# Performance work log

Measured on AMD Instinct MI355X. Metric: run time of the kernel, lower is better.

## Reference

```python
import jax, jax.numpy as jnp
import numpy as np

D_MODEL = 1024
D_STATE = 16
D_CONV = 4
EXPAND = 2
D_INNER = EXPAND * D_MODEL          # 2048
DT_RANK = (D_MODEL + 15) // 16      # 64 (mamba 'auto')
B, L = 2, 1024


def _mamba_params(key, scale=0.02):
    ks = jax.random.split(key, 6)
    return dict(
        inW=jax.random.normal(ks[0], (2 * D_INNER, D_MODEL), jnp.float32) * scale,
        convW=jax.random.normal(ks[1], (D_INNER, 1, D_CONV), jnp.float32) * scale,
        convb=jnp.zeros((D_INNER,), jnp.float32),
        xprojW=jax.random.normal(ks[2], (DT_RANK + 2 * D_STATE, D_INNER), jnp.float32) * scale,
        dtW=jax.random.normal(ks[3], (D_INNER, DT_RANK), jnp.float32) * scale,
        dtb=jax.random.normal(ks[4], (D_INNER,), jnp.float32) * scale,
        A_log=jnp.log(jnp.tile(jnp.arange(1, D_STATE + 1, dtype=jnp.float32), (D_INNER, 1))),
        Dskip=jnp.ones((D_INNER,), jnp.float32),
        outW=jax.random.normal(ks[5], (D_MODEL, D_INNER), jnp.float32) * scale,
    )


def setup_inputs() -> dict:
    key = jax.random.key(0)
    kx, kf, kb, kp = jax.random.split(key, 4)
    inp = {"x": jax.random.normal(kx, (B, L, D_MODEL), jnp.float32)}
    inp["ln_w"] = jnp.ones((D_MODEL,), jnp.float32)
    inp["ln_b"] = jnp.zeros((D_MODEL,), jnp.float32)
    for pref, k in (("f_", kf), ("b_", kb)):
        for name, v in _mamba_params(k).items():
            inp[pref + name] = v
    inp["proj_W"] = jax.random.normal(kp, (D_MODEL, 2 * D_MODEL), jnp.float32) * 0.02
    inp["proj_b"] = jnp.zeros((D_MODEL,), jnp.float32)
    return inp


def _layernorm(x, w, b, eps=1e-5):
    mu = jnp.mean(x, axis=-1, keepdims=True)
    var = jnp.var(x, axis=-1, keepdims=True)
    return (x - mu) * jax.lax.rsqrt(var + eps) * w + b


def _mamba(x, inW, convW, convb, xprojW, dtW, dtb, A_log, Dskip, outW):
    # x: [B, L, d_model]
    xz = jnp.einsum('bld,ed->ble', x, inW)           # [B,L,2*d_inner]
    xs, z = jnp.split(xz, 2, axis=-1)                # each [B,L,d_inner]
    # depthwise causal conv over L
    xc = jnp.transpose(xs, (0, 2, 1))                # [B,d_inner,L]
    xc = jax.lax.conv_general_dilated(
        xc, convW, window_strides=(1,), padding=[(D_CONV - 1, 0)],
        feature_group_count=D_INNER)
    xs = jax.nn.silu(jnp.transpose(xc + convb[None, :, None], (0, 2, 1)))
    # input-dependent dt, B, C
    xdb = jnp.einsum('bld,ed->ble', xs, xprojW)      # [B,L,dt_rank+2*d_state]
    dt, Bm, Cm = jnp.split(xdb, [DT_RANK, DT_RANK + D_STATE], axis=-1)
    dt = jax.nn.softplus(jnp.einsum('blr,dr->bld', dt, dtW) + dtb)  # [B,L,d_inner]
    A = -jnp.exp(A_log)                              # [d_inner,d_state], negative
    dA = jnp.exp(dt[..., None] * A)                  # [B,L,d_inner,d_state]
    dBx = dt[..., None] * Bm[:, :, None, :] * xs[..., None]

    def step(h, inputs):
        dA_t, dBx_t, C_t = inputs                    # [B,d,s],[B,d,s],[B,s]
        h = h * dA_t + dBx_t
        y = jnp.einsum('bds,bs->bd', h, C_t)
        return h, y

    h0 = jnp.zeros((x.shape[0], D_INNER, D_STATE), x.dtype)
    _, ys = jax.lax.scan(step, h0, (jnp.moveaxis(dA, 1, 0),
                                    jnp.moveaxis(dBx, 1, 0),
                                    jnp.moveaxis(Cm, 1, 0)))
    y = jnp.moveaxis(ys, 0, 1)                       # [B,L,d_inner]
    y = (y + xs * Dskip) * jax.nn.silu(z)
    return jnp.einsum('bld,ed->ble', y, outW)        # [B,L,d_model]


def reference(x, ln_w, ln_b,
              f_inW, f_convW, f_convb, f_xprojW, f_dtW, f_dtb, f_A_log, f_Dskip, f_outW,
              b_inW, b_convW, b_convb, b_xprojW, b_dtW, b_dtb, b_A_log, b_Dskip, b_outW,
              proj_W, proj_b):
    normed = _layernorm(x, ln_w, ln_b)
    fwd_out = _mamba(normed, f_inW, f_convW, f_convb, f_xprojW, f_dtW, f_dtb,
                     f_A_log, f_Dskip, f_outW)
    bwd_out = _mamba(normed[:, ::-1, :], b_inW, b_convW, b_convb, b_xprojW, b_dtW,
                     b_dtb, b_A_log, b_Dskip, b_outW)[:, ::-1, :]
    combined = jnp.concatenate([fwd_out, bwd_out], axis=-1)
    return x + jnp.einsum('blc,ec->ble', combined, proj_W) + proj_b
```

## Files before the change

kernel.cpp:

```cpp
#include <hip/hip_runtime.h>
#include <hip/hip_bf16.h>
#include <math.h>

#define DM   1024
#define DI   2048
#define DTR  64
#define DST  16
#define NB   2
#define LL   1024
#define MR   (NB*LL)
#define XLD  128
#define KS   8

typedef __bf16 bf16x8 __attribute__((ext_vector_type(8)));
typedef float  f32x4  __attribute__((ext_vector_type(4)));
typedef unsigned short u16x8 __attribute__((ext_vector_type(8)));

__device__ __forceinline__ float siluf(float x) { return x / (1.f + __expf(-x)); }
__device__ __forceinline__ float softplusf(float x) {
    return fmaxf(x, 0.f) + log1pf(__expf(-fabsf(x)));
}
__device__ __forceinline__ unsigned short f2bf(float f) {
    __hip_bfloat16 h = __float2bfloat16(f);
    return *reinterpret_cast<unsigned short*>(&h);
}
__device__ __forceinline__ float bf2f(__hip_bfloat16 h) { return __bfloat162float(h); }
__device__ __forceinline__ float bfu2f(unsigned short u) {
    __hip_bfloat16 h = *reinterpret_cast<__hip_bfloat16*>(&u);
    return __bfloat162float(h);
}

__device__ __forceinline__ void gl2lds16(const __hip_bfloat16* g, __hip_bfloat16* l)
{
    __builtin_amdgcn_global_load_lds(
        (const __attribute__((address_space(1))) unsigned int*)g,
        (__attribute__((address_space(3))) unsigned int*)l, 16, 0, 0);
}

__global__ __launch_bounds__(256) void prep_k(
    const float* __restrict__ s0, const float* __restrict__ s1,
    const float* __restrict__ s2, const float* __restrict__ s3,
    const float* __restrict__ s4, __hip_bfloat16* __restrict__ warena,
    const float* __restrict__ fx, const float* __restrict__ bx,
    __hip_bfloat16* __restrict__ wpb2,
    const float* __restrict__ fo, const float* __restrict__ bo,
    __hip_bfloat16* __restrict__ wot,
    const float* __restrict__ x, const float* __restrict__ lnw,
    const float* __restrict__ lnb, __hip_bfloat16* __restrict__ nb)
{
    __shared__ float pshm[64 * 65];
    const int b = blockIdx.x;
    const int tid = threadIdx.x;

    if (b < 2624) {
        long base = (long)b * 4096;
        const float* src; long off;
        if      (base <  4194304L) { src = s0; off = base; }
        else if (base <  8388608L) { src = s1; off = base -  4194304L; }
        else if (base < 10485760L) { src = s2; off = base -  8388608L; }
        else if (base < 10616832L) { src = s3; off = base - 10485760L; }
        else                       { src = s4; off = base - 10616832L; }
        #pragma unroll
        for (int j = 0; j < 4; ++j) {
            long e = (long)j * 1024 + tid * 4;
            float4 v = *(const float4*)(src + off + e);
            ushort4 o;
            o.x = f2bf(v.x); o.y = f2bf(v.y); o.z = f2bf(v.z); o.w = f2bf(v.w);
            *(ushort4*)((unsigned short*)warena + base + e) = o;
        }
    } else if (b < 2752) {
        int t = b - 2624;
        int z = t >> 6;
        const float* in = z ? bx : fx;
        int idx = ((t & 63) * 256 + tid) * 4;
        int row = idx >> 11;
        ushort4 o = make_ushort4(0, 0, 0, 0);
        if (row < 96) {
            float4 v = *(const float4*)(in + idx);
            o.x = f2bf(v.x); o.y = f2bf(v.y); o.z = f2bf(v.z); o.w = f2bf(v.w);
        }
        *(ushort4*)((unsigned short*)wpb2 + (size_t)z * 128 * DI + idx) = o;
    } else if (b < 3776) {
        int t = b - 2752;
        int z = t >> 9; t &= 511;
        const float* src = z ? bo : fo;
        int c0 = (t & 31) * 64;
        int r0 = (t >> 5) * 64;
        int tc = tid & 63;
        int tr = tid >> 6;
        #pragma unroll
        for (int ii = 0; ii < 16; ++ii) {
            int rl = tr + ii * 4;
            pshm[tc * 65 + rl] = src[(size_t)(r0 + rl) * DI + c0 + tc];
        }
        __syncthreads();
        __hip_bfloat16* dst = wot + (size_t)z * DI * DM;
        #pragma unroll
        for (int ii = 0; ii < 16; ++ii) {
            int cl = tr + ii * 4;
            dst[(size_t)(c0 + cl) * DM + r0 + tc] = __float2bfloat16(pshm[cl * 65 + tc]);
        }
    } else {
        int row = b - 3776;
        const float* xr = x + (size_t)row * DM;
        float4 v = *(const float4*)(xr + tid * 4);
        float s = v.x + v.y + v.z + v.w;
        float q = v.x*v.x + v.y*v.y + v.z*v.z + v.w*v.w;
        #pragma unroll
        for (int off = 32; off > 0; off >>= 1) {
            s += __shfl_xor(s, off, 64);
            q += __shfl_xor(q, off, 64);
        }
        int wv = tid >> 6;
        if ((tid & 63) == 0) { pshm[wv] = s; pshm[8 + wv] = q; }
        __syncthreads();
        s = pshm[0] + pshm[1] + pshm[2] + pshm[3];
        q = pshm[8] + pshm[9] + pshm[10] + pshm[11];
        float mu  = s * (1.f / DM);
        float var = q * (1.f / DM) - mu * mu;
        float rstd = rsqrtf(var + 1e-5f);
        float4 wv4 = *(const float4*)(lnw + tid * 4);
        float4 bv4 = *(const float4*)(lnb + tid * 4);
        ushort4 o;
        o.x = f2bf((v.x - mu) * rstd * wv4.x + bv4.x);
        o.y = f2bf((v.y - mu) * rstd * wv4.y + bv4.y);
        o.z = f2bf((v.z - mu) * rstd * wv4.z + bv4.z);
        o.w = f2bf((v.w - mu) * rstd * wv4.w + bv4.w);
        *(ushort4*)((unsigned short*)nb + (size_t)row * DM + tid * 4) = o;
    }
}

__global__ __launch_bounds__(512) void inproj256_k(
    const __hip_bfloat16* __restrict__ A,
    const __hip_bfloat16* __restrict__ Bmat,
    __hip_bfloat16* __restrict__ C)
{
    __shared__ __hip_bfloat16 smem[65536];
    const int tid = threadIdx.x;
    int id = blockIdx.x;
    int s  = (id & 7) * 32 + (id >> 3);
    const int z  = s >> 7;
    const int r  = s & 127;
    const int bm = (r & 7) * 256;
    const int bn = (r >> 3) * 256;
    const __hip_bfloat16* Az = A;
    const __hip_bfloat16* Bz = Bmat + (size_t)z * 2 * DI * DM;
    __hip_bfloat16* Cz = C + (size_t)z * MR * 2 * DI;

    const int wv   = tid >> 6;
    const int lane = tid & 63;
    const int wm   = wv >> 2;
    const int wn   = wv & 3;
    const int fr   = lane & 15;
    const int quad = lane >> 4;

    const int srow = tid >> 2;
    const int scol = 8 * ((tid & 3) ^ ((tid >> 3) & 3));
    const int kph  = (quad ^ ((fr >> 1) & 3)) * 8;

    __hip_bfloat16* const Asl = smem;
    __hip_bfloat16* const Bsl = smem + 32768;

    f32x4 acc[8][4] = {};
    bf16x8 aF[4], bB[4];

#define STG_A(TAU, KK) { \
    const int ub_ = (((TAU) & 1) * 2 + (KK)) * 8192; \
    const int gc_ = (TAU) * 64 + (KK) * 32 + scol; \
    gl2lds16(Az + (size_t)(bm + srow) * DM + gc_,       Asl + ub_ + tid * 8); \
    gl2lds16(Az + (size_t)(bm + 128 + srow) * DM + gc_, Asl + ub_ + 4096 + tid * 8); }
#define STG_B(TAU, KK) { \
    const int ub_ = (((TAU) & 1) * 2 + (KK)) * 8192; \
    const int gc_ = (TAU) * 64 + (KK) * 32 + scol; \
    gl2lds16(Bz + (size_t)(bn + srow) * DM + gc_,       Bsl + ub_ + tid * 8); \
    gl2lds16(Bz + (size_t)(bn + 128 + srow) * DM + gc_, Bsl + ub_ + 4096 + tid * 8); }

#define RD_A(BUF, KK, MH) { \
    const __hip_bfloat16* p_ = Asl + ((BUF) * 2 + (KK)) * 8192 + kph; \
    _Pragma("unroll") for (int i = 0; i < 4; ++i) \
        aF[i] = *(const bf16x8*)(p_ + (wm * 128 + (MH) * 64 + i * 16 + fr) * 32); }
#define RD_B(BUF, KK) { \
    const __hip_bfloat16* p_ = Bsl + ((BUF) * 2 + (KK)) * 8192 + kph; \
    _Pragma("unroll") for (int j = 0; j < 4; ++j) \
        bB[j] = *(const bf16x8*)(p_ + (wn * 64 + j * 16 + fr) * 32); }

#define PHASE(BUF, KK, MH, STGC, T1, T2, VMC) { \
    if ((MH) == 0) { RD_B(BUF, KK); } \
    RD_A(BUF, KK, MH); \
    if ((STGC) == 1) { STG_A((T1), 1); } \
    if ((STGC) == 2) { STG_B((T1), 1); } \
    if ((STGC) == 3) { STG_A((T2), 0); } \
    if ((STGC) == 4) { STG_B((T2), 0); } \
    asm volatile("s_barrier" ::: "memory"); \
    asm volatile("s_waitcnt lgkmcnt(0)" ::: "memory"); \
    __builtin_amdgcn_sched_barrier(0); \
    __builtin_amdgcn_s_setprio(1); \
    _Pragma("unroll") for (int i = 0; i < 4; ++i) \
        _Pragma("unroll") for (int j = 0; j < 4; ++j) \
            acc[(MH) * 4 + i][j] = __builtin_amdgcn_mfma_f32_16x16x32_bf16( \
                aF[i], bB[j], acc[(MH) * 4 + i][j], 0, 0, 0); \
    __builtin_amdgcn_s_setprio(0); \
    if ((VMC) == 8) { asm volatile("s_waitcnt vmcnt(8)" ::: "memory"); } \
    if ((VMC) == 4) { asm volatile("s_waitcnt vmcnt(4)" ::: "memory"); } \
    if ((VMC) == 1) { asm volatile("s_waitcnt vmcnt(0)" ::: "memory"); } \
    asm volatile("s_barrier" ::: "memory"); }

    STG_A(0, 0); STG_B(0, 0); STG_A(0, 1); STG_B(0, 1); STG_A(1, 0); STG_B(1, 0);
    asm volatile("s_waitcnt vmcnt(8)" ::: "memory");
    asm volatile("s_barrier" ::: "memory");

    #pragma unroll 1
    for (int t = 0; t < 14; ++t) {
        const int buf = t & 1;
        const int t1 = t + 1, t2 = t + 2;
        PHASE(buf, 0, 0, 1, t1, t2, 0);
        PHASE(buf, 0, 1, 2, t1, t2, 8);
        PHASE(buf, 1, 0, 3, t1, t2, 0);
        PHASE(buf, 1, 1, 4, t1, t2, 8);
    }
    PHASE(0, 0, 0, 1, 15, 0, 0);
    PHASE(0, 0, 1, 2, 15, 0, 8);
    PHASE(0, 1, 0, 0, 0, 0, 0);
    PHASE(0, 1, 1, 0, 0, 0, 4);
    PHASE(1, 0, 0, 0, 0, 0, 0);
    PHASE(1, 0, 1, 0, 0, 0, 1);
    PHASE(1, 1, 0, 0, 0, 0, 0);
    PHASE(1, 1, 1, 0, 0, 0, 0);

#undef PHASE
#undef RD_A
#undef RD_B
#undef STG_A
#undef STG_B

    float* eps = (float*)smem;
    const int orow = tid >> 3;
    const int ocol = (tid & 7) * 32;
    #pragma unroll
    for (int p = 0; p < 4; ++p) {
        __syncthreads();
        if (wm == (p >> 1)) {
            int ib = (p & 1) * 4;
            #pragma unroll
            for (int i2 = 0; i2 < 4; ++i2)
                #pragma unroll
                for (int j = 0; j < 4; ++j)
                    #pragma unroll
                    for (int rr = 0; rr < 4; ++rr)
                        eps[(i2 * 16 + quad * 4 + rr) * 260 + wn * 64 + j * 16 + fr]
                            = acc[ib + i2][j][rr];
        }
        __syncthreads();
        unsigned short os[32] __attribute__((aligned(16)));
        #pragma unroll
        for (int c = 0; c < 32; ++c) os[c] = f2bf(eps[orow * 260 + ocol + c]);
        unsigned short* dst = (unsigned short*)Cz +
            (size_t)(bm + p * 64 + orow) * (2 * DI) + bn + ocol;
        *(uint4*)(dst +  0) = *(const uint4*)(os +  0);
        *(uint4*)(dst +  8) = *(const uint4*)(os +  8);
        *(uint4*)(dst + 16) = *(const uint4*)(os + 16);
        *(uint4*)(dst + 24) = *(const uint4*)(os + 24);
    }
}

template<int EPI>
__global__ __launch_bounds__(256) void gemm_gl(
    const __hip_bfloat16* __restrict__ A, int lda, size_t aofs,
    const __hip_bfloat16* __restrict__ B, int ldb, size_t bofs,
    void* __restrict__ Cp, int ldc, size_t cofs, int K,
    const float* __restrict__ bias0, const float* __restrict__ bias1)
{
    __shared__ __hip_bfloat16 smem[2 * 128 * 64];
    __hip_bfloat16* As = smem;
    __hip_bfloat16* Bs = smem + 128 * 64;
    const int tid  = threadIdx.x;
    const int z    = blockIdx.z;
    const int bm   = blockIdx.y * 128;
    const int bn   = blockIdx.x * 128;
    const __hip_bfloat16* Az = A + (size_t)z * aofs;
    const __hip_bfloat16* Bz = B + (size_t)z * bofs;
    const int wv   = tid >> 6;
    const int lane = tid & 63;
    const int wr   = (wv >> 1) * 64;
    const int wc   = (wv & 1) * 64;
    const int srow = wv * 32 + (lane >> 3);
    const int cg   = ((lane & 7) ^ (lane >> 3)) * 8;
    const int fr   = lane & 15;
    const int quad = lane >> 4;
    const int pc0  = (quad ^ (fr & 7)) * 8;
    const int pc1  = ((4 + quad) ^ (fr & 7)) * 8;

    f32x4 acc[4][4] = {};

    for (int k0 = 0; k0 < K; k0 += 64) {
        __syncthreads();
        #pragma unroll
        for (int i = 0; i < 4; ++i) {
            int r = srow + i * 8;
            gl2lds16(Az + (size_t)(bm + r) * lda + k0 + cg, As + wv * 2048 + i * 512);
            gl2lds16(Bz + (size_t)(bn + r) * ldb + k0 + cg, Bs + wv * 2048 + i * 512);
        }
        __syncthreads();
        #pragma unroll
        for (int kk = 0; kk < 2; ++kk) {
            const int pc = kk ? pc1 : pc0;
            bf16x8 af[4], bf_[4];
            #pragma unroll
            for (int i = 0; i < 4; ++i) {
                af[i]  = *(const bf16x8*)(As + (wr + i * 16 + fr) * 64 + pc);
                bf_[i] = *(const bf16x8*)(Bs + (wc + i * 16 + fr) * 64 + pc);
            }
            #pragma unroll
            for (int i = 0; i < 4; ++i)
                #pragma unroll
                for (int j = 0; j < 4; ++j)
                    acc[i][j] = __builtin_amdgcn_mfma_f32_16x16x32_bf16(
                        af[i], bf_[j], acc[i][j], 0, 0, 0);
        }
    }

    const float* bias = (EPI == 3) ? (z ? bias1 : bias0) : nullptr;
    float* eps = (float*)smem;
    const int half = wv >> 1;
    const int lrow = tid >> 3;
    const int cseg = (tid & 7) * 16;
    const int gr_  = bm + (lrow >> 4) * 64 + (lrow & 15);
    #pragma unroll
    for (int i = 0; i < 4; ++i) {
        __syncthreads();
        #pragma unroll
        for (int j = 0; j < 4; ++j)
            #pragma unroll
            for (int r = 0; r < 4; ++r)
                eps[(half * 16 + quad * 4 + r) * 132 + wc + j * 16 + fr] = acc[i][j][r];
        __syncthreads();
        float vals[16];
        *(float4*)(vals +  0) = *(const float4*)(eps + lrow * 132 + cseg +  0);
        *(float4*)(vals +  4) = *(const float4*)(eps + lrow * 132 + cseg +  4);
        *(float4*)(vals +  8) = *(const float4*)(eps + lrow * 132 + cseg +  8);
        *(float4*)(vals + 12) = *(const float4*)(eps + lrow * 132 + cseg + 12);
        int gr = gr_ + i * 16;
        int gc = bn + cseg;
        unsigned short os[16];
        #pragma unroll
        for (int c = 0; c < 16; ++c) {
            float t = vals[c];
            if (EPI == 3) t = softplusf(t + bias[gc + c]);
            os[c] = f2bf(t);
        }
        unsigned short* dst = (unsigned short*)Cp + (size_t)z * cofs +
                              (size_t)gr * ldc + gc;
        *(ushort4*)(dst +  0) = *(ushort4*)(os +  0);
        *(ushort4*)(dst +  4) = *(ushort4*)(os +  4);
        *(ushort4*)(dst +  8) = *(ushort4*)(os +  8);
        *(ushort4*)(dst + 12) = *(ushort4*)(os + 12);
    }
}

__global__ __launch_bounds__(256) void conv_wcat_k(
    const __hip_bfloat16* __restrict__ xz2,
    const float* __restrict__ fW, const float* __restrict__ fb,
    const float* __restrict__ bW, const float* __restrict__ bb_,
    __hip_bfloat16* __restrict__ xsb2,
    const __hip_bfloat16* __restrict__ pwb,
    const __hip_bfloat16* __restrict__ wot,
    __hip_bfloat16* __restrict__ wcat)
{
    __shared__ __hip_bfloat16 smem[2 * 128 * 64];
    const int b   = blockIdx.x;
    const int tid = threadIdx.x;

    if (b < 1024) {
        const int dirv  = b >> 9;
        const int chunk = b & 511;
        const int bb    = chunk >> 8;
        const int t0    = (chunk & 255) * 4;
        const int d     = tid * 8;

        const float* w    = (dirv ? bW : fW) + d * 4;
        const float* bias = (dirv ? bb_ : fb) + d;
        const unsigned short* xz =
            (const unsigned short*)(xz2 + (size_t)dirv * MR * 2 * DI) + d;

        u16x8 rows[7];
        #pragma unroll
        for (int rr = 0; rr < 7; ++rr) {
            int t = dirv ? (t0 + rr) : (t0 - 3 + rr);
            bool ok = dirv ? (t < LL) : (t >= 0);
            u16x8 v = {};
            if (ok) v = *(const u16x8*)(xz + (size_t)(bb * LL + t) * (2 * DI));
            rows[rr] = v;
        }
        float wq[8][4];
        #pragma unroll
        for (int c = 0; c < 8; ++c) {
            float4 t = *(const float4*)(w + c * 4);
            if (dirv) { wq[c][0]=t.w; wq[c][1]=t.z; wq[c][2]=t.y; wq[c][3]=t.x; }
            else      { wq[c][0]=t.x; wq[c][1]=t.y; wq[c][2]=t.z; wq[c][3]=t.w; }
        }
        float4 b0 = *(const float4*)(bias);
        float4 b1 = *(const float4*)(bias + 4);
        float bs[8] = {b0.x, b0.y, b0.z, b0.w, b1.x, b1.y, b1.z, b1.w};

        unsigned short* outp = (unsigned short*)xsb2 + (size_t)dirv * MR * DI +
                               (size_t)(bb * LL + t0) * DI + d;
        #pragma unroll
        for (int o = 0; o < 4; ++o) {
            unsigned short os[8] __attribute__((aligned(16)));
            #pragma unroll
            for (int c = 0; c < 8; ++c) {
                float a = bs[c];
                #pragma unroll
                for (int k = 0; k < 4; ++k)
                    a = fmaf(wq[c][k], bfu2f(rows[o + k][c]), a);
                os[c] = f2bf(siluf(a));
            }
            *(uint4*)(outp + (size_t)o * DI) = *(const uint4*)os;
        }
        return;
    }

    const int t_   = b - 1024;
    const int bn   = (t_ & 15) * 128;
    const int bm   = ((t_ >> 4) & 7) * 128;
    const int z    = t_ >> 7;
    const __hip_bfloat16* Az = pwb + (size_t)z * DM;
    const __hip_bfloat16* Bz = wot + (size_t)z * DI * DM;
    __hip_bfloat16* As = smem;
    __hip_bfloat16* Bs = smem + 128 * 64;
    const int wv   = tid >> 6;
    const int lane = tid & 63;
    const int wr   = (wv >> 1) * 64;
    const int wc   = (wv & 1) * 64;
    const int srow = wv * 32 + (lane >> 3);
    const int cg   = ((lane & 7) ^ (lane >> 3)) * 8;
    const int fr   = lane & 15;
    const int quad = lane >> 4;
    const int pc0  = (quad ^ (fr & 7)) * 8;
    const int pc1  = ((4 + quad) ^ (fr & 7)) * 8;

    f32x4 acc[4][4] = {};

    for (int k0 = 0; k0 < DM; k0 += 64) {
        __syncthreads();
        #pragma unroll
        for (int i = 0; i < 4; ++i) {
            int r = srow + i * 8;
            gl2lds16(Az + (size_t)(bm + r) * (2 * DM) + k0 + cg, As + wv * 2048 + i * 512);
            gl2lds16(Bz + (size_t)(bn + r) * DM + k0 + cg,       Bs + wv * 2048 + i * 512);
        }
        __syncthreads();
        #pragma unroll
        for (int kk = 0; kk < 2; ++kk) {
            const int pc = kk ? pc1 : pc0;
            bf16x8 af[4], bf_[4];
            #pragma unroll
            for (int i = 0; i < 4; ++i) {
                af[i]  = *(const bf16x8*)(As + (wr + i * 16 + fr) * 64 + pc);
                bf_[i] = *(const bf16x8*)(Bs + (wc + i * 16 + fr) * 64 + pc);
            }
            #pragma unroll
            for (int i = 0; i < 4; ++i)
                #pragma unroll
                for (int j = 0; j < 4; ++j)
                    acc[i][j] = __builtin_amdgcn_mfma_f32_16x16x32_bf16(
                        af[i], bf_[j], acc[i][j], 0, 0, 0);
        }
    }

    float* eps = (float*)smem;
    const int half = wv >> 1;
    const int lrow = tid >> 3;
    const int cseg = (tid & 7) * 16;
    const int gr_  = bm + (lrow >> 4) * 64 + (lrow & 15);
    #pragma unroll
    for (int i = 0; i < 4; ++i) {
        __syncthreads();
        #pragma unroll
        for (int j = 0; j < 4; ++j)
            #pragma unroll
            for (int r = 0; r < 4; ++r)
                eps[(half * 16 + quad * 4 + r) * 132 + wc + j * 16 + fr] = acc[i][j][r];
        __syncthreads();
        float vals[16];
        *(float4*)(vals +  0) = *(const float4*)(eps + lrow * 132 + cseg +  0);
        *(float4*)(vals +  4) = *(const float4*)(eps + lrow * 132 + cseg +  4);
        *(float4*)(vals +  8) = *(const float4*)(eps + lrow * 132 + cseg +  8);
        *(float4*)(vals + 12) = *(const float4*)(eps + lrow * 132 + cseg + 12);
        int gr = gr_ + i * 16;
        int gc = bn + cseg;
        unsigned short os[16];
        #pragma unroll
        for (int c = 0; c < 16; ++c) os[c] = f2bf(vals[c]);
        unsigned short* dst = (unsigned short*)wcat + (size_t)z * DI +
                              (size_t)gr * (2 * DI) + gc;
        *(ushort4*)(dst +  0) = *(ushort4*)(os +  0);
        *(ushort4*)(dst +  4) = *(ushort4*)(os +  4);
        *(ushort4*)(dst +  8) = *(ushort4*)(os +  8);
        *(ushort4*)(dst + 12) = *(ushort4*)(os + 12);
    }
}

__global__ __launch_bounds__(256) void outproj_k(
    const __hip_bfloat16* __restrict__ A,
    const __hip_bfloat16* __restrict__ Bm,
    const float* __restrict__ x, const float* __restrict__ proj_b,
    float* __restrict__ out)
{
    __shared__ __hip_bfloat16 smem[2 * 64 * 64];
    __hip_bfloat16* As = smem;
    __hip_bfloat16* Bs = smem + 64 * 64;
    const int tid  = threadIdx.x;
    const int bn   = blockIdx.x * 64;
    const int bm   = blockIdx.y * 64;
    const int wv   = tid >> 6;
    const int lane = tid & 63;
    const int wr   = (wv >> 1) * 32;
    const int wc   = (wv & 1) * 32;
    const int srow = wv * 16 + (lane >> 3);
    const int cg   = ((lane & 7) ^ (lane >> 3)) * 8;
    const int fr   = lane & 15;
    const int quad = lane >> 4;
    const int pc0  = (quad ^ (fr & 7)) * 8;
    const int pc1  = ((4 + quad) ^ (fr & 7)) * 8;
    const int K    = 2 * DI;

    f32x4 acc[2][2] = {};

    for (int k0 = 0; k0 < K; k0 += 64) {
        __syncthreads();
        #pragma unroll
        for (int j = 0; j < 2; ++j) {
            int r = srow + j * 8;
            gl2lds16(A  + (size_t)(bm + r) * K + k0 + cg, As + wv * 1024 + j * 512);
            gl2lds16(Bm + (size_t)(bn + r) * K + k0 + cg, Bs + wv * 1024 + j * 512);
        }
        __syncthreads();
        #pragma unroll
        for (int kk = 0; kk < 2; ++kk) {
            const int pc = kk ? pc1 : pc0;
            bf16x8 af[2], bf_[2];
            #pragma unroll
            for (int i = 0; i < 2; ++i) {
                af[i]  = *(const bf16x8*)(As + (wr + i * 16 + fr) * 64 + pc);
                bf_[i] = *(const bf16x8*)(Bs + (wc + i * 16 + fr) * 64 + pc);
            }
            #pragma unroll
            for (int i = 0; i < 2; ++i)
                #pragma unroll
                for (int j = 0; j < 2; ++j)
                    acc[i][j] = __builtin_amdgcn_mfma_f32_16x16x32_bf16(
                        af[i], bf_[j], acc[i][j], 0, 0, 0);
        }
    }

    const float pb0 = proj_b[bn + wc + fr];
    const float pb1 = proj_b[bn + wc + 16 + fr];
    #pragma unroll
    for (int i = 0; i < 2; ++i)
        #pragma unroll
        for (int j = 0; j < 2; ++j) {
            const int gc = bn + wc + j * 16 + fr;
            const float pb = j ? pb1 : pb0;
            #pragma unroll
            for (int r = 0; r < 4; ++r) {
                size_t off = (size_t)(bm + wr + i * 16 + quad * 4 + r) * DM + gc;
                out[off] = x[off] + pb + acc[i][j][r];
            }
        }
}

__global__ __launch_bounds__(256) void xproj_part_k(
    const __hip_bfloat16* __restrict__ A,
    const __hip_bfloat16* __restrict__ B,
    float* __restrict__ part)
{
    __shared__ __hip_bfloat16 smem[2 * 128 * 64];
    __hip_bfloat16* As = smem;
    __hip_bfloat16* Bs = smem + 128 * 64;
    const int tid  = threadIdx.x;
    const int ks   = blockIdx.x;
    const int bm   = blockIdx.y * 128;
    const int z    = blockIdx.z;
    const __hip_bfloat16* Az = A + (size_t)z * MR * DI;
    const __hip_bfloat16* Bz = B + (size_t)z * 128 * DI;
    const int kb   = ks * (DI / KS);
    const int wv   = tid >> 6;
    const int lane = tid & 63;
    const int wr   = (wv >> 1) * 64;
    const int wc   = (wv & 1) * 64;
    const int srow = wv * 32 + (lane >> 3);
    const int cg   = ((lane & 7) ^ (lane >> 3)) * 8;
    const int fr   = lane & 15;
    const int quad = lane >> 4;
    const int pc0  = (quad ^ (fr & 7)) * 8;
    const int pc1  = ((4 + quad) ^ (fr & 7)) * 8;

    f32x4 acc[4][4] = {};

    #pragma unroll
    for (int k0 = 0; k0 < DI / KS; k0 += 64) {
        __syncthreads();
        #pragma unroll
        for (int i = 0; i < 4; ++i) {
            int r = srow + i * 8;
            gl2lds16(Az + (size_t)(bm + r) * DI + kb + k0 + cg, As + wv * 2048 + i * 512);
            gl2lds16(Bz + (size_t)r * DI + kb + k0 + cg,        Bs + wv * 2048 + i * 512);
        }
        __syncthreads();
        #pragma unroll
        for (int kk = 0; kk < 2; ++kk) {
            const int pc = kk ? pc1 : pc0;
            bf16x8 af[4], bf_[4];
            #pragma unroll
            for (int i = 0; i < 4; ++i) {
                af[i]  = *(const bf16x8*)(As + (wr + i * 16 + fr) * 64 + pc);
                bf_[i] = *(const bf16x8*)(Bs + (wc + i * 16 + fr) * 64 + pc);
            }
            #pragma unroll
            for (int i = 0; i < 4; ++i)
                #pragma unroll
                for (int j = 0; j < 4; ++j)
                    acc[i][j] = __builtin_amdgcn_mfma_f32_16x16x32_bf16(
                        af[i], bf_[j], acc[i][j], 0, 0, 0);
        }
    }

    float* dst = part + ((size_t)z * KS + ks) * MR * XLD;
    const int er = quad * 4;
    #pragma unroll
    for (int i = 0; i < 4; ++i)
        #pragma unroll
        for (int j = 0; j < 4; ++j) {
            int row = bm + wr + i * 16 + er;
            int col = wc + j * 16 + fr;
            #pragma unroll
            for (int r = 0; r < 4; ++r)
                dst[(size_t)(row + r) * XLD + col] = acc[i][j][r];
        }
}

__global__ __launch_bounds__(256) void xproj_reduce_k(
    const float* __restrict__ part, float* __restrict__ xdb,
    __hip_bfloat16* __restrict__ xdbt)
{
    int z = blockIdx.y;
    size_t idx = ((size_t)blockIdx.x * 256 + threadIdx.x) * 4;
    const float* p = part + (size_t)z * KS * MR * XLD;
    float4 s = make_float4(0.f, 0.f, 0.f, 0.f);
    #pragma unroll
    for (int ks = 0; ks < KS; ++ks) {
        float4 v = *(const float4*)(p + (size_t)ks * MR * XLD + idx);
        s.x += v.x; s.y += v.y; s.z += v.z; s.w += v.w;
    }
    *(float4*)(xdb + (size_t)z * MR * XLD + idx) = s;
    int c = (int)(idx & (XLD - 1));
    if (c < 64) {
        size_t m = idx >> 7;
        ushort4 o;
        o.x = f2bf(s.x); o.y = f2bf(s.y); o.z = f2bf(s.z); o.w = f2bf(s.w);
        *(ushort4*)((unsigned short*)xdbt + (size_t)z * MR * 64 + m * 64 + c) = o;
    }
}

__global__ __launch_bounds__(256) void conv_silu_k(
    const __hip_bfloat16* __restrict__ xz2,
    const float* __restrict__ fW, const float* __restrict__ fb,
    const float* __restrict__ bW, const float* __restrict__ bb_,
    __hip_bfloat16* __restrict__ xsb2)
{
    const int dirv  = blockIdx.y;
    const int chunk = blockIdx.x;
    const int bb    = chunk >> 8;
    const int t0    = (chunk & 255) * 4;
    const int d     = threadIdx.x * 8;

    const float* w    = (dirv ? bW : fW) + d * 4;
    const float* bias = (dirv ? bb_ : fb) + d;
    const unsigned short* xz =
        (const unsigned short*)(xz2 + (size_t)dirv * MR * 2 * DI) + d;

    u16x8 rows[7];
    #pragma unroll
    for (int rr = 0; rr < 7; ++rr) {
        int t = dirv ? (t0 + rr) : (t0 - 3 + rr);
        bool ok = dirv ? (t < LL) : (t >= 0);
        u16x8 v = {};
        if (ok) v = *(const u16x8*)(xz + (size_t)(bb * LL + t) * (2 * DI));
        rows[rr] = v;
    }
    float wq[8][4];
    #pragma unroll
    for (int c = 0; c < 8; ++c) {
        float4 t = *(const float4*)(w + c * 4);
        if (dirv) { wq[c][0]=t.w; wq[c][1]=t.z; wq[c][2]=t.y; wq[c][3]=t.x; }
        else      { wq[c][0]=t.x; wq[c][1]=t.y; wq[c][2]=t.z; wq[c][3]=t.w; }
    }
    float4 b0 = *(const float4*)(bias);
    float4 b1 = *(const float4*)(bias + 4);
    float bs[8] = {b0.x, b0.y, b0.z, b0.w, b1.x, b1.y, b1.z, b1.w};

    unsigned short* outp = (unsigned short*)xsb2 + (size_t)dirv * MR * DI +
                           (size_t)(bb * LL + t0) * DI + d;
    #pragma unroll
    for (int o = 0; o < 4; ++o) {
        unsigned short os[8] __attribute__((aligned(16)));
        #pragma unroll
        for (int c = 0; c < 8; ++c) {
            float a = bs[c];
            #pragma unroll
            for (int k = 0; k < 4; ++k)
                a = fmaf(wq[c][k], bfu2f(rows[o + k][c]), a);
            os[c] = f2bf(siluf(a));
        }
        *(uint4*)(outp + (size_t)o * DI) = *(const uint4*)os;
    }
}

__global__ __launch_bounds__(256) void scan1_k(
    const __hip_bfloat16* __restrict__ dtf2, const __hip_bfloat16* __restrict__ xsb2,
    const float* __restrict__ xdb2,
    const float* __restrict__ fA, const float* __restrict__ bA,
    float* __restrict__ hend, float* __restrict__ aprod, int G, int Cn)
{
    int d  = blockIdx.x * 256 + threadIdx.x;
    int bb = blockIdx.y;
    int zz = blockIdx.z;
    int dirv = (zz >= G) ? 1 : 0;
    int g = zz - (dirv ? G : 0);
    const float* A_log = dirv ? bA : fA;
    const __hip_bfloat16* dtf = dtf2 + (size_t)dirv * MR * DI;
    const __hip_bfloat16* xs = xsb2 + (size_t)dirv * MR * DI;
    const float* xdb = xdb2 + (size_t)dirv * MR * XLD;
    size_t hoff = (size_t)dirv * G * (NB * DI * DST);

    float Ad[DST], h[DST], ap[DST];
    bool pw = true;
    #pragma unroll
    for (int s = 0; s < DST; ++s) {
        Ad[s] = -__expf(A_log[d * DST + s]);
        pw = pw && (fabsf(Ad[s] + (float)(s + 1)) < 1e-3f * (s + 1));
        h[s] = 0.f; ap[s] = 1.f;
    }
    int i0 = g * Cn;
    for (int i = 0; i < Cn; ++i) {
        int ii = i0 + i;
        int t = dirv ? (LL - 1 - ii) : ii;
        size_t m = (size_t)bb * LL + t;
        float dtv = bf2f(dtf[m * DI + d]);
        float xv  = bf2f(xs[m * DI + d]);
        const float* bc = xdb + m * XLD;
        float dtx = dtv * xv;
        float dAv[DST];
        if (pw) {
            float r = __expf(-dtv);
            float a = r;
            #pragma unroll
            for (int s = 0; s < DST; ++s) { dAv[s] = a; a *= r; }
        } else {
            #pragma unroll
            for (int s = 0; s < DST; ++s) dAv[s] = __expf(dtv * Ad[s]);
        }
        #pragma unroll
        for (int s = 0; s < DST; ++s) {
            h[s] = fmaf(h[s], dAv[s], dtx * bc[64 + s]);
            ap[s] *= dAv[s];
        }
    }
    size_t base = hoff + ((size_t)(g * NB + bb) * DI + d) * DST;
    #pragma unroll
    for (int s = 0; s < DST; s += 4) {
        *(float4*)(hend  + base + s) = make_float4(h[s], h[s+1], h[s+2], h[s+3]);
        *(float4*)(aprod + base + s) = make_float4(ap[s], ap[s+1], ap[s+2], ap[s+3]);
    }
}

__global__ __launch_bounds__(256) void scan2_k(
    float* __restrict__ hend, const float* __restrict__ aprod, int G)
{
    int dirv = blockIdx.y;
    int idx = blockIdx.x * 256 + threadIdx.x;
    const int slab = NB * DI * DST;
    size_t hoff = (size_t)dirv * G * slab;
    float carry = 0.f;
    for (int g = 0; g < G; ++g) {
        size_t off = hoff + (size_t)g * slab + idx;
        float a = aprod[off];
        float e = hend[off];
        hend[off] = carry;
        carry = fmaf(a, carry, e);
    }
}

__global__ __launch_bounds__(256) void scan3_k(
    const __hip_bfloat16* __restrict__ dtf2, const __hip_bfloat16* __restrict__ xsb2,
    const float* __restrict__ xdb2, const __hip_bfloat16* __restrict__ xz2,
    const float* __restrict__ fA, const float* __restrict__ bA,
    const float* __restrict__ fD, const float* __restrict__ bD,
    const float* __restrict__ hin, __hip_bfloat16* __restrict__ ycat, int G, int Cn)
{
    int d  = blockIdx.x * 256 + threadIdx.x;
    int bb = blockIdx.y;
    int zz = blockIdx.z;
    int dirv = (zz >= G) ? 1 : 0;
    int g = zz - (dirv ? G : 0);
    const float* A_log = dirv ? bA : fA;
    const float* Dskip = dirv ? bD : fD;
    const __hip_bfloat16* dtf = dtf2 + (size_t)dirv * MR * DI;
    const __hip_bfloat16* xs = xsb2 + (size_t)dirv * MR * DI;
    const float* xdb = xdb2 + (size_t)dirv * MR * XLD;
    const __hip_bfloat16* xz = xz2 + (size_t)dirv * MR * 2 * DI;
    size_t hoff = (size_t)dirv * G * (NB * DI * DST);

    float Ad[DST], h[DST];
    bool pw = true;
    size_t base = hoff + ((size_t)(g * NB + bb) * DI + d) * DST;
    #pragma unroll
    for (int s = 0; s < DST; ++s) {
        Ad[s] = -__expf(A_log[d * DST + s]);
        pw = pw && (fabsf(Ad[s] + (float)(s + 1)) < 1e-3f * (s + 1));
        h[s] = hin[base + s];
    }
    float Dsk = Dskip[d];
    int i0 = g * Cn;
    for (int i = 0; i < Cn; ++i) {
        int ii = i0 + i;
        int t = dirv ? (LL - 1 - ii) : ii;
        size_t m = (size_t)bb * LL + t;
        float dtv = bf2f(dtf[m * DI + d]);
        float xv  = bf2f(xs[m * DI + d]);
        const float* bc = xdb + m * XLD;
        float dtx = dtv * xv;
        float dAv[DST];
        if (pw) {
            float r = __expf(-dtv);
            float a = r;
            #pragma unroll
            for (int s = 0; s < DST; ++s) { dAv[s] = a; a *= r; }
        } else {
            #pragma unroll
            for (int s = 0; s < DST; ++s) dAv[s] = __expf(dtv * Ad[s]);
        }
        float yv = 0.f;
        #pragma unroll
        for (int s = 0; s < DST; ++s) {
            h[s] = fmaf(h[s], dAv[s], dtx * bc[64 + s]);
            yv = fmaf(h[s], bc[80 + s], yv);
        }
        float zv = bf2f(xz[m * (2 * DI) + DI + d]);
        ycat[m * (2 * DI) + (size_t)dirv * DI + d] =
            __float2bfloat16((yv + xv * Dsk) * siluf(zv));
    }
}

__global__ __launch_bounds__(256) void scan_mono_k(
    const __hip_bfloat16* __restrict__ dtf2, const __hip_bfloat16* __restrict__ xsb2,
    const float* __restrict__ xdb2, const __hip_bfloat16* __restrict__ xz2,
    const float* __restrict__ fA, const float* __restrict__ bA,
    const float* __restrict__ fD, const float* __restrict__ bD,
    __hip_bfloat16* __restrict__ ycat)
{
    int d  = blockIdx.x * 256 + threadIdx.x;
    int bb = blockIdx.y;
    int dirv = blockIdx.z;
    const float* A_log = dirv ? bA : fA;
    const float* Dskip = dirv ? bD : fD;
    const __hip_bfloat16* dtf = dtf2 + (size_t)dirv * MR * DI;
    const __hip_bfloat16* xs = xsb2 + (size_t)dirv * MR * DI;
    const float* xdb = xdb2 + (size_t)dirv * MR * XLD;
    const __hip_bfloat16* xz = xz2 + (size_t)dirv * MR * 2 * DI;
    float Ad[DST], h[DST];
    #pragma unroll
    for (int s = 0; s < DST; ++s) { Ad[s] = -__expf(A_log[d * DST + s]); h[s] = 0.f; }
    float Dsk = Dskip[d];
    for (int i = 0; i < LL; ++i) {
        int t = dirv ? (LL - 1 - i) : i;
        size_t m = (size_t)bb * LL + t;
        float dtv = bf2f(dtf[m * DI + d]);
        float xv  = bf2f(xs[m * DI + d]);
        const float* bc = xdb + m * XLD;
        float dtx = dtv * xv;
        float yv = 0.f;
        #pragma unroll
        for (int s = 0; s < DST; ++s) {
            float dA = __expf(dtv * Ad[s]);
            h[s] = fmaf(h[s], dA, dtx * bc[64 + s]);
            yv = fmaf(h[s], bc[80 + s], yv);
        }
        float zv = bf2f(xz[m * (2 * DI) + DI + d]);
        ycat[m * (2 * DI) + (size_t)dirv * DI + d] =
            __float2bfloat16((yv + xv * Dsk) * siluf(zv));
    }
}

extern "C" void kernel_launch(void* const* d_in, const int* in_sizes, int n_in,
                              void* d_out, int out_size, void* d_ws, size_t ws_size,
                              hipStream_t stream)
{
    const float* x      = (const float*)d_in[0];
    const float* ln_w   = (const float*)d_in[1];
    const float* ln_b   = (const float*)d_in[2];
    const float* f_inW    = (const float*)d_in[3];
    const float* f_convW  = (const float*)d_in[4];
    const float* f_convb  = (const float*)d_in[5];
    const float* f_xprojW = (const float*)d_in[6];
    const float* f_dtW    = (const float*)d_in[7];
    const float* f_dtb    = (const float*)d_in[8];
    const float* f_A_log  = (const float*)d_in[9];
    const float* f_Dskip  = (const float*)d_in[10];
    const float* f_outW   = (const float*)d_in[11];
    const float* b_inW    = (const float*)d_in[12];
    const float* b_convW  = (const float*)d_in[13];
    const float* b_convb  = (const float*)d_in[14];
    const float* b_xprojW = (const float*)d_in[15];
    const float* b_dtW    = (const float*)d_in[16];
    const float* b_dtb    = (const float*)d_in[17];
    const float* b_A_log  = (const float*)d_in[18];
    const float* b_Dskip  = (const float*)d_in[19];
    const float* b_outW   = (const float*)d_in[20];
    const float* proj_W = (const float*)d_in[21];
    const float* proj_b = (const float*)d_in[22];

    float* ws = (float*)d_ws;
    size_t o = 0;
    __hip_bfloat16* xz2  = (__hip_bfloat16*)(ws + o);
    o += (size_t)2 * MR * 2 * DI / 2;
    __hip_bfloat16* xsb2 = (__hip_bfloat16*)(ws + o); o += (size_t)2 * MR * DI / 2;
    __hip_bfloat16* ycat = (__hip_bfloat16*)(ws + o);
    float* xpart = ws + o;
    o += (size_t)MR * 2 * DI / 2;
    float* xdb2 = ws + o; o += (size_t)2 * MR * XLD;
    __hip_bfloat16* xdbt = (__hip_bfloat16*)(ws + o); o += (size_t)2 * MR * 64 / 2;
    __hip_bfloat16* dtfb = (__hip_bfloat16*)(ws + o); o += (size_t)2 * MR * DI / 2;
    __hip_bfloat16* nb = (__hip_bfloat16*)(ws + o); o += (size_t)MR * DM / 2;
    __hip_bfloat16* warena = (__hip_bfloat16*)(ws + o); o += 15466496 / 2;
    float* hbuf = ws + o;
    size_t base_floats = o;

    __hip_bfloat16* wbi  = warena;
    __hip_bfloat16* pwb  = warena +  8388608;
    __hip_bfloat16* wdt  = warena + 10485760;
    __hip_bfloat16* wpb2 = warena + 10747904;
    __hip_bfloat16* wcat = warena + 11272192;

    const size_t slab = (size_t)NB * DI * DST;
    int G = 32;
    while (G > 4 && (base_floats + 4ull * G * slab) * 4 > ws_size) G >>= 1;
    int useChunks = ((base_floats + 4ull * G * slab) * 4 <= ws_size);
    float* hend  = hbuf;
    float* aprod = hbuf + 2ull * G * slab;
    int Cn = useChunks ? LL / G : LL;

    int wotInHbuf = useChunks && (4ull * G * slab >= 2097152ull);
    __hip_bfloat16* wot = wotInHbuf ? (__hip_bfloat16*)hbuf : xz2;

    prep_k<<<5824, 256, 0, stream>>>(
        f_inW, b_inW, proj_W, f_dtW, b_dtW, warena,
        f_xprojW, b_xprojW, wpb2,
        f_outW, b_outW, wot,
        x, ln_w, ln_b, nb);

    if (wotInHbuf) {
        inproj256_k<<<256, 512, 0, stream>>>(nb, wbi, xz2);
        conv_wcat_k<<<1280, 256, 0, stream>>>(
            xz2, f_convW, f_convb, b_convW, b_convb, xsb2, pwb, wot, wcat);
    } else {
        gemm_gl<1><<<dim3(DI / 128, DM / 128, 2), 256, 0, stream>>>(
            pwb, 2 * DM, (size_t)DM, wot, DM, (size_t)DI * DM,
            wcat, 2 * DI, (size_t)DI, DM, nullptr, nullptr);
        inproj256_k<<<256, 512, 0, stream>>>(nb, wbi, xz2);
        conv_silu_k<<<dim3(MR / 4, 2), 256, 0, stream>>>(
            xz2, f_convW, f_convb, b_convW, b_convb, xsb2);
    }

    xproj_part_k<<<dim3(KS, MR / 128, 2), 256, 0, stream>>>(xsb2, wpb2, xpart);
    xproj_reduce_k<<<dim3((MR * XLD) / 1024, 2), 256, 0, stream>>>(xpart, xdb2, xdbt);

    gemm_gl<3><<<dim3(DI / 128, MR / 128, 2), 256, 0, stream>>>(
        xdbt, 64, (size_t)MR * 64, wdt, 64, (size_t)DI * 64,
        dtfb, DI, (size_t)MR * DI, 64, f_dtb, b_dtb);

    if (useChunks) {
        scan1_k<<<dim3(DI / 256, NB, 2 * G), 256, 0, stream>>>(
            dtfb, xsb2, xdb2, f_A_log, b_A_log, hend, aprod, G, Cn);
        scan2_k<<<dim3((NB * DI * DST) / 256, 2), 256, 0, stream>>>(hend, aprod, G);
        scan3_k<<<dim3(DI / 256, NB, 2 * G), 256, 0, stream>>>(
            dtfb, xsb2, xdb2, xz2, f_A_log, b_A_log, f_Dskip, b_Dskip,
            hend, ycat, G, Cn);
    } else {
        scan_mono_k<<<dim3(DI / 256, NB, 2), 256, 0, stream>>>(
            dtfb, xsb2, xdb2, xz2, f_A_log, b_A_log, f_Dskip, b_Dskip, ycat);
    }

    outproj_k<<<dim3(DM / 64, MR / 64), 256, 0, stream>>>(
        ycat, wcat, x, proj_b, (float*)d_out);
}
```

Baseline: 387.6 us.

## Replace split-K x_proj GEMM plus reduction with single small-M-tile kernel

Replaces the split-K x_proj GEMM (8 K-slices writing fp32 partials) and its separate reduction kernel with one kernel. It tiles M by 32 rows and loops over the full K=2048, writing the fp32 result and the bf16 dt slice directly. This removes the partial-buffer traffic (about 16 MB written and read) and one launch. In exchange the kernel has 128 blocks with a long serial K loop, no double buffering, and reloads the full 128-row B tile for each block.

Result: slower. 404.3 us (+4.3%).

```diff
diff --git a/kernel.cpp b/kernel.cpp
--- a/kernel.cpp
+++ b/kernel.cpp
@@ -10,7 +10,6 @@
 #define LL   1024
 #define MR   (NB*LL)
 #define XLD  128
-#define KS   8
 
 typedef __bf16 bf16x8 __attribute__((ext_vector_type(8)));
 typedef float  f32x4  __attribute__((ext_vector_type(4)));
@@ -501,6 +500,69 @@
     }
 }
 
+__global__ __launch_bounds__(256) void xproj64_k(
+    const __hip_bfloat16* __restrict__ A,
+    const __hip_bfloat16* __restrict__ B,
+    float* __restrict__ xdb,
+    __hip_bfloat16* __restrict__ xdbt)
+{
+    __shared__ __hip_bfloat16 smem[(32 + 128) * 64];
+    __hip_bfloat16* As = smem;
+    __hip_bfloat16* Bs = smem + 32 * 64;
+    const int tid = threadIdx.x;
+    const int z   = blockIdx.y;
+    const int bm  = blockIdx.x * 32;
+    const __hip_bfloat16* Az = A + (size_t)z * MR * DI;
+    const __hip_bfloat16* Bz = B + (size_t)z * 128 * DI;
+    const int wv   = tid >> 6;
+    const int lane = tid & 63;
+    const int wm   = wv >> 1;
+    const int wn   = wv & 1;
+    const int fr   = lane & 15;
+    const int quad = lane >> 4;
+    const int srow = tid >> 3;
+    const int cg   = ((tid & 7) ^ (srow & 7)) * 8;
+    const int pc0  = (quad ^ (fr & 7)) * 8;
+    const int pc1  = ((4 + quad) ^ (fr & 7)) * 8;
+
+    f32x4 acc[4] = {};
+
+    for (int k0 = 0; k0 < DI; k0 += 64) {
+        __syncthreads();
+        gl2lds16(Az + (size_t)(bm + srow) * DI + k0 + cg, As + tid * 8);
+        #pragma unroll
+        for (int i = 0; i < 4; ++i)
+            gl2lds16(Bz + (size_t)(i * 32 + srow) * DI + k0 + cg,
+                     Bs + i * 2048 + tid * 8);
+        __syncthreads();
+        #pragma unroll
+        for (int kk = 0; kk < 2; ++kk) {
+            const int pc = kk ? pc1 : pc0;
+            bf16x8 af = *(const bf16x8*)(As + (wm * 16 + fr) * 64 + pc);
+            #pragma unroll
+            for (int j = 0; j < 4; ++j) {
+                bf16x8 bf_ = *(const bf16x8*)(Bs + (wn * 64 + j * 16 + fr) * 64 + pc);
+                acc[j] = __builtin_amdgcn_mfma_f32_16x16x32_bf16(af, bf_, acc[j], 0, 0, 0);
+            }
+        }
+    }
+
+    float* xdbz = xdb + (size_t)z * MR * XLD;
+    unsigned short* xdtz = (unsigned short*)xdbt + (size_t)z * MR * 64;
+    #pragma unroll
+    for (int j = 0; j < 4; ++j) {
+        const int col = wn * 64 + j * 16 + fr;
+        #pragma unroll
+        for (int r = 0; r < 4; ++r) {
+            const int row = bm + wm * 16 + quad * 4 + r;
+            const float v = acc[j][r];
+            xdbz[(size_t)row * XLD + col] = v;
+            if (wn == 0)
+                xdtz[(size_t)row * 64 + col] = f2bf(v);
+        }
+    }
+}
+
 __global__ __launch_bounds__(256) void outproj_k(
     const __hip_bfloat16* __restrict__ A,
     const __hip_bfloat16* __restrict__ Bm,
@@ -568,99 +630,6 @@
                 out[off] = x[off] + pb + acc[i][j][r];
             }
         }
-}
-
-__global__ __launch_bounds__(256) void xproj_part_k(
-    const __hip_bfloat16* __restrict__ A,
-    const __hip_bfloat16* __restrict__ B,
-    float* __restrict__ part)
-{
-    __shared__ __hip_bfloat16 smem[2 * 128 * 64];
-    __hip_bfloat16* As = smem;
-    __hip_bfloat16* Bs = smem + 128 * 64;
-    const int tid  = threadIdx.x;
-    const int ks   = blockIdx.x;
-    const int bm   = blockIdx.y * 128;
-    const int z    = blockIdx.z;
-    const __hip_bfloat16* Az = A + (size_t)z * MR * DI;
-    const __hip_bfloat16* Bz = B + (size_t)z * 128 * DI;
-    const int kb   = ks * (DI / KS);
-    const int wv   = tid >> 6;
-    const int lane = tid & 63;
-    const int wr   = (wv >> 1) * 64;
-    const int wc   = (wv & 1) * 64;
-    const int srow = wv * 32 + (lane >> 3);
-    const int cg   = ((lane & 7) ^ (lane >> 3)) * 8;
-    const int fr   = lane & 15;
-    const int quad = lane >> 4;
-    const int pc0  = (quad ^ (fr & 7)) * 8;
-    const int pc1  = ((4 + quad) ^ (fr & 7)) * 8;
-
-    f32x4 acc[4][4] = {};
-
-    #pragma unroll
-    for (int k0 = 0; k0 < DI / KS; k0 += 64) {
-        __syncthreads();
-        #pragma unroll
-        for (int i = 0; i < 4; ++i) {
-            int r = srow + i * 8;
-            gl2lds16(Az + (size_t)(bm + r) * DI + kb + k0 + cg, As + wv * 2048 + i * 512);
-            gl2lds16(Bz + (size_t)r * DI + kb + k0 + cg,        Bs + wv * 2048 + i * 512);
-        }
-        __syncthreads();
-        #pragma unroll
-        for (int kk = 0; kk < 2; ++kk) {
-            const int pc = kk ? pc1 : pc0;
-            bf16x8 af[4], bf_[4];
-            #pragma unroll
-            for (int i = 0; i < 4; ++i) {
-                af[i]  = *(const bf16x8*)(As + (wr + i * 16 + fr) * 64 + pc);
-                bf_[i] = *(const bf16x8*)(Bs + (wc + i * 16 + fr) * 64 + pc);
-            }
-            #pragma unroll
-            for (int i = 0; i < 4; ++i)
-                #pragma unroll
-                for (int j = 0; j < 4; ++j)
-                    acc[i][j] = __builtin_amdgcn_mfma_f32_16x16x32_bf16(
-                        af[i], bf_[j], acc[i][j], 0, 0, 0);
-        }
-    }
-
-    float* dst = part + ((size_t)z * KS + ks) * MR * XLD;
-    const int er = quad * 4;
-    #pragma unroll
-    for (int i = 0; i < 4; ++i)
-        #pragma unroll
-        for (int j = 0; j < 4; ++j) {
-            int row = bm + wr + i * 16 + er;
-            int col = wc + j * 16 + fr;
-            #pragma unroll
-            for (int r = 0; r < 4; ++r)
-                dst[(size_t)(row + r) * XLD + col] = acc[i][j][r];
-        }
-}
-
-__global__ __launch_bounds__(256) void xproj_reduce_k(
-    const float* __restrict__ part, float* __restrict__ xdb,
-    __hip_bfloat16* __restrict__ xdbt)
-{
-    int z = blockIdx.y;
-    size_t idx = ((size_t)blockIdx.x * 256 + threadIdx.x) * 4;
-    const float* p = part + (size_t)z * KS * MR * XLD;
-    float4 s = make_float4(0.f, 0.f, 0.f, 0.f);
-    #pragma unroll
-    for (int ks = 0; ks < KS; ++ks) {
-        float4 v = *(const float4*)(p + (size_t)ks * MR * XLD + idx);
-        s.x += v.x; s.y += v.y; s.z += v.z; s.w += v.w;
-    }
-    *(float4*)(xdb + (size_t)z * MR * XLD + idx) = s;
-    int c = (int)(idx & (XLD - 1));
-    if (c < 64) {
-        size_t m = idx >> 7;
-        ushort4 o;
-        o.x = f2bf(s.x); o.y = f2bf(s.y); o.z = f2bf(s.z); o.w = f2bf(s.w);
-        *(ushort4*)((unsigned short*)xdbt + (size_t)z * MR * 64 + m * 64 + c) = o;
-    }
 }
 
 __global__ __launch_bounds__(256) void conv_silu_k(
@@ -927,7 +896,6 @@
     o += (size_t)2 * MR * 2 * DI / 2;
     __hip_bfloat16* xsb2 = (__hip_bfloat16*)(ws + o); o += (size_t)2 * MR * DI / 2;
     __hip_bfloat16* ycat = (__hip_bfloat16*)(ws + o);
-    float* xpart = ws + o;
     o += (size_t)MR * 2 * DI / 2;
     float* xdb2 = ws + o; o += (size_t)2 * MR * XLD;
     __hip_bfloat16* xdbt = (__hip_bfloat16*)(ws + o); o += (size_t)2 * MR * 64 / 2;
@@ -973,8 +941,7 @@
             xz2, f_convW, f_convb, b_convW, b_convb, xsb2);
     }
 
-    xproj_part_k<<<dim3(KS, MR / 128, 2), 256, 0, stream>>>(xsb2, wpb2, xpart);
-    xproj_reduce_k<<<dim3((MR * XLD) / 1024, 2), 256, 0, stream>>>(xpart, xdb2, xdbt);
+    xproj64_k<<<dim3(MR / 32, 2), 256, 0, stream>>>(xsb2, wpb2, xdb2, xdbt);
 
     gemm_gl<3><<<dim3(DI / 128, MR / 128, 2), 256, 0, stream>>>(
         xdbt, 64, (size_t)MR * 64, wdt, 64, (size_t)DI * 64,
```

## Shrink in-projection GEMM tile to 256x128 and drop hand-scheduled pipeline

Applied to the files above, without the earlier changes.

The in-projection GEMM goes from 256x256 tiles with a hand-tuned, double-buffered, phase-interleaved schedule to 256x128 tiles with a simple single-buffered loop: load a K=64 slab into LDS, sync, then run MFMAs. The grid doubles to 512 blocks and LDS use drops sharply, which may allow more blocks per CU and better CU fill. The cost is lost overlap between global loads and MFMA, lower per-block reuse of the A tile, and narrower epilogue stores.

Measured after the change: 374.9 us. 3.3% less time.

```diff
diff --git a/kernel.cpp b/kernel.cpp
--- a/kernel.cpp
+++ b/kernel.cpp
@@ -135,131 +135,94 @@
     const __hip_bfloat16* __restrict__ Bmat,
     __hip_bfloat16* __restrict__ C)
 {
-    __shared__ __hip_bfloat16 smem[65536];
+    __shared__ __hip_bfloat16 smem[24576];
+    __hip_bfloat16* const As = smem;
+    __hip_bfloat16* const Bs = smem + 16384;
     const int tid = threadIdx.x;
     int id = blockIdx.x;
-    int s  = (id & 7) * 32 + (id >> 3);
-    const int z  = s >> 7;
-    const int r  = s & 127;
+    int s  = (id & 7) * 64 + (id >> 3);
+    const int z  = s >> 8;
+    const int r  = s & 255;
     const int bm = (r & 7) * 256;
-    const int bn = (r >> 3) * 256;
+    const int bn = (r >> 3) * 128;
     const __hip_bfloat16* Az = A;
     const __hip_bfloat16* Bz = Bmat + (size_t)z * 2 * DI * DM;
     __hip_bfloat16* Cz = C + (size_t)z * MR * 2 * DI;
 
     const int wv   = tid >> 6;
     const int lane = tid & 63;
-    const int wm   = wv >> 2;
-    const int wn   = wv & 3;
+    const int wm   = wv >> 1;
+    const int wn   = wv & 1;
     const int fr   = lane & 15;
     const int quad = lane >> 4;
-
-    const int srow = tid >> 2;
-    const int scol = 8 * ((tid & 3) ^ ((tid >> 3) & 3));
-    const int kph  = (quad ^ ((fr >> 1) & 3)) * 8;
-
-    __hip_bfloat16* const Asl = smem;
-    __hip_bfloat16* const Bsl = smem + 32768;
-
-    f32x4 acc[8][4] = {};
-    bf16x8 aF[4], bB[4];
-
-#define STG_A(TAU, KK) { \
-    const int ub_ = (((TAU) & 1) * 2 + (KK)) * 8192; \
-    const int gc_ = (TAU) * 64 + (KK) * 32 + scol; \
-    gl2lds16(Az + (size_t)(bm + srow) * DM + gc_,       Asl + ub_ + tid * 8); \
-    gl2lds16(Az + (size_t)(bm + 128 + srow) * DM + gc_, Asl + ub_ + 4096 + tid * 8); }
-#define STG_B(TAU, KK) { \
-    const int ub_ = (((TAU) & 1) * 2 + (KK)) * 8192; \
-    const int gc_ = (TAU) * 64 + (KK) * 32 + scol; \
-    gl2lds16(Bz + (size_t)(bn + srow) * DM + gc_,       Bsl + ub_ + tid * 8); \
-    gl2lds16(Bz + (size_t)(bn + 128 + srow) * DM + gc_, Bsl + ub_ + 4096 + tid * 8); }
-
-#define RD_A(BUF, KK, MH) { \
-    const __hip_bfloat16* p_ = Asl + ((BUF) * 2 + (KK)) * 8192 + kph; \
-    _Pragma("unroll") for (int i = 0; i < 4; ++i) \
-        aF[i] = *(const bf16x8*)(p_ + (wm * 128 + (MH) * 64 + i * 16 + fr) * 32); }
-#define RD_B(BUF, KK) { \
-    const __hip_bfloat16* p_ = Bsl + ((BUF) * 2 + (KK)) * 8192 + kph; \
-    _Pragma("unroll") for (int j = 0; j < 4; ++j) \
-        bB[j] = *(const bf16x8*)(p_ + (wn * 64 + j * 16 + fr) * 32); }
-
-#define PHASE(BUF, KK, MH, STGC, T1, T2, VMC) { \
-    if ((MH) == 0) { RD_B(BUF, KK); } \
-    RD_A(BUF, KK, MH); \
-    if ((STGC) == 1) { STG_A((T1), 1); } \
-    if ((STGC) == 2) { STG_B((T1), 1); } \
-    if ((STGC) == 3) { STG_A((T2), 0); } \
-    if ((STGC) == 4) { STG_B((T2), 0); } \
-    asm volatile("s_barrier" ::: "memory"); \
-    asm volatile("s_waitcnt lgkmcnt(0)" ::: "memory"); \
-    __builtin_amdgcn_sched_barrier(0); \
-    __builtin_amdgcn_s_setprio(1); \
-    _Pragma("unroll") for (int i = 0; i < 4; ++i) \
-        _Pragma("unroll") for (int j = 0; j < 4; ++j) \
-            acc[(MH) * 4 + i][j] = __builtin_amdgcn_mfma_f32_16x16x32_bf16( \
-                aF[i], bB[j], acc[(MH) * 4 + i][j], 0, 0, 0); \
-    __builtin_amdgcn_s_setprio(0); \
-    if ((VMC) == 8) { asm volatile("s_waitcnt vmcnt(8)" ::: "memory"); } \
-    if ((VMC) == 4) { asm volatile("s_waitcnt vmcnt(4)" ::: "memory"); } \
-    if ((VMC) == 1) { asm volatile("s_waitcnt vmcnt(0)" ::: "memory"); } \
-    asm volatile("s_barrier" ::: "memory"); }
-
-    STG_A(0, 0); STG_B(0, 0); STG_A(0, 1); STG_B(0, 1); STG_A(1, 0); STG_B(1, 0);
-    asm volatile("s_waitcnt vmcnt(8)" ::: "memory");
-    asm volatile("s_barrier" ::: "memory");
-
-    #pragma unroll 1
-    for (int t = 0; t < 14; ++t) {
-        const int buf = t & 1;
-        const int t1 = t + 1, t2 = t + 2;
-        PHASE(buf, 0, 0, 1, t1, t2, 0);
-        PHASE(buf, 0, 1, 2, t1, t2, 8);
-        PHASE(buf, 1, 0, 3, t1, t2, 0);
-        PHASE(buf, 1, 1, 4, t1, t2, 8);
-    }
-    PHASE(0, 0, 0, 1, 15, 0, 0);
-    PHASE(0, 0, 1, 2, 15, 0, 8);
-    PHASE(0, 1, 0, 0, 0, 0, 0);
-    PHASE(0, 1, 1, 0, 0, 0, 4);
-    PHASE(1, 0, 0, 0, 0, 0, 0);
-    PHASE(1, 0, 1, 0, 0, 0, 1);
-    PHASE(1, 1, 0, 0, 0, 0, 0);
-    PHASE(1, 1, 1, 0, 0, 0, 0);
-
-#undef PHASE
-#undef RD_A
-#undef RD_B
-#undef STG_A
-#undef STG_B
+    const int sr8  = tid >> 3;
+    const int cg   = ((tid & 7) ^ (sr8 & 7)) * 8;
+
+    f32x4 acc[4][4] = {};
+
+    for (int k0 = 0; k0 < DM; k0 += 64) {
+        __syncthreads();
+        #pragma unroll
+        for (int i = 0; i < 4; ++i)
+            gl2lds16(Az + (size_t)(bm + sr8 + i * 64) * DM + k0 + cg,
+                     As + i * 4096 + tid * 8);
+        #pragma unroll
+        for (int i = 0; i < 2; ++i)
+            gl2lds16(Bz + (size_t)(bn + sr8 + i * 64) * DM + k0 + cg,
+                     Bs + i * 4096 + tid * 8);
+        __syncthreads();
+        #pragma unroll
+        for (int kk = 0; kk < 2; ++kk) {
+            const int pc = ((kk * 4 + quad) ^ (fr & 7)) * 8;
+            bf16x8 af[4], bf_[4];
+            #pragma unroll
+            for (int i = 0; i < 4; ++i)
+                af[i]  = *(const bf16x8*)(As + (wm * 64 + i * 16 + fr) * 64 + pc);
+            #pragma unroll
+            for (int j = 0; j < 4; ++j)
+                bf_[j] = *(const bf16x8*)(Bs + (wn * 64 + j * 16 + fr) * 64 + pc);
+            __builtin_amdgcn_s_setprio(1);
+            #pragma unroll
+            for (int i = 0; i < 4; ++i)
+                #pragma unroll
+                for (int j = 0; j < 4; ++j)
+                    acc[i][j] = __builtin_amdgcn_mfma_f32_16x16x32_bf16(
+                        af[i], bf_[j], acc[i][j], 0, 0, 0);
+            __builtin_amdgcn_s_setprio(0);
+        }
+    }
 
     float* eps = (float*)smem;
     const int orow = tid >> 3;
-    const int ocol = (tid & 7) * 32;
+    const int ocol = (tid & 7) * 16;
     #pragma unroll
     for (int p = 0; p < 4; ++p) {
         __syncthreads();
-        if (wm == (p >> 1)) {
-            int ib = (p & 1) * 4;
-            #pragma unroll
-            for (int i2 = 0; i2 < 4; ++i2)
+        if (wm == p) {
+            #pragma unroll
+            for (int i = 0; i < 4; ++i)
                 #pragma unroll
                 for (int j = 0; j < 4; ++j)
                     #pragma unroll
                     for (int rr = 0; rr < 4; ++rr)
-                        eps[(i2 * 16 + quad * 4 + rr) * 260 + wn * 64 + j * 16 + fr]
-                            = acc[ib + i2][j][rr];
-        }
-        __syncthreads();
-        unsigned short os[32] __attribute__((aligned(16)));
-        #pragma unroll
-        for (int c = 0; c < 32; ++c) os[c] = f2bf(eps[orow * 260 + ocol + c]);
+                        eps[(i * 16 + quad * 4 + rr) * 132 + wn * 64 + j * 16 + fr]
+                            = acc[i][j][rr];
+        }
+        __syncthreads();
+        float vals[16];
+        *(float4*)(vals +  0) = *(const float4*)(eps + orow * 132 + ocol +  0);
+        *(float4*)(vals +  4) = *(const float4*)(eps + orow * 132 + ocol +  4);
+        *(float4*)(vals +  8) = *(const float4*)(eps + orow * 132 + ocol +  8);
+        *(float4*)(vals + 12) = *(const float4*)(eps + orow * 132 + ocol + 12);
+        unsigned short os[16] __attribute__((aligned(16)));
+        #pragma unroll
+        for (int c = 0; c < 16; ++c) os[c] = f2bf(vals[c]);
         unsigned short* dst = (unsigned short*)Cz +
             (size_t)(bm + p * 64 + orow) * (2 * DI) + bn + ocol;
-        *(uint4*)(dst +  0) = *(const uint4*)(os +  0);
-        *(uint4*)(dst +  8) = *(const uint4*)(os +  8);
-        *(uint4*)(dst + 16) = *(const uint4*)(os + 16);
-        *(uint4*)(dst + 24) = *(const uint4*)(os + 24);
+        *(ushort4*)(dst +  0) = *(ushort4*)(os +  0);
+        *(ushort4*)(dst +  4) = *(ushort4*)(os +  4);
+        *(ushort4*)(dst +  8) = *(ushort4*)(os +  8);
+        *(ushort4*)(dst + 12) = *(ushort4*)(os + 12);
     }
 }
 
@@ -961,14 +924,14 @@
         x, ln_w, ln_b, nb);
 
     if (wotInHbuf) {
-        inproj256_k<<<256, 512, 0, stream>>>(nb, wbi, xz2);
+        inproj256_k<<<512, 512, 0, stream>>>(nb, wbi, xz2);
         conv_wcat_k<<<1280, 256, 0, stream>>>(
             xz2, f_convW, f_convb, b_convW, b_convb, xsb2, pwb, wot, wcat);
     } else {
         gemm_gl<1><<<dim3(DI / 128, DM / 128, 2), 256, 0, stream>>>(
             pwb, 2 * DM, (size_t)DM, wot, DM, (size_t)DI * DM,
             wcat, 2 * DI, (size_t)DI, DM, nullptr, nullptr);
-        inproj256_k<<<256, 512, 0, stream>>>(nb, wbi, xz2);
+        inproj256_k<<<512, 512, 0, stream>>>(nb, wbi, xz2);
         conv_silu_k<<<dim3(MR / 4, 2), 256, 0, stream>>>(
             xz2, f_convW, f_convb, b_convW, b_convb, xsb2);
     }
```
